# Optimization experiments

Measured on AMD Instinct MI355X. Metric: run time of the kernel, lower is better.

## Reference

```python
import jax, jax.numpy as jnp
import numpy as np

N_X, DIS, IN, OUT = 40000, 10000, 128, 64
N = N_X + DIS
E = 800000
BN_EPS = 1e-5


def setup_inputs() -> dict:
    key = jax.random.key(0)
    ks = jax.random.split(key, 20)

    def glorot(k, shape):
        fan_in, fan_out = shape[-2], shape[-1]
        a = np.sqrt(6.0 / (fan_in + fan_out)).astype(np.float32)
        return jax.random.uniform(k, shape, jnp.float32, -a, a)

    return {
        "x": jax.random.normal(ks[0], (N_X, IN), jnp.float32),
        "emb": jax.random.uniform(ks[1], (DIS, IN), jnp.float32),
        "conv1_w": glorot(ks[2], (3, IN, 2 * OUT)),
        "conv1_root": glorot(ks[3], (IN, 2 * OUT)),
        "conv1_bias": jnp.zeros((2 * OUT,), jnp.float32),
        "conv2_w": glorot(ks[4], (3, 2 * OUT, 4 * OUT)),
        "conv2_root": glorot(ks[5], (2 * OUT, 4 * OUT)),
        "conv2_bias": jnp.zeros((4 * OUT,), jnp.float32),
        "convinf_w": glorot(ks[6], (3, 4 * OUT, 4 * OUT)),
        "convinf_root": glorot(ks[7], (4 * OUT, 4 * OUT)),
        "convinf_bias": jnp.zeros((4 * OUT,), jnp.float32),
        "conv3_w": glorot(ks[8], (3, 4 * OUT, OUT)),
        "conv3_root": glorot(ks[9], (4 * OUT, OUT)),
        "conv3_bias": jnp.zeros((OUT,), jnp.float32),
        "norm1_g": jnp.ones((2 * OUT,), jnp.float32),
        "norm1_b": jnp.zeros((2 * OUT,), jnp.float32),
        "norm2_g": jnp.ones((4 * OUT,), jnp.float32),
        "norm2_b": jnp.zeros((4 * OUT,), jnp.float32),
        "edge_index": jax.random.randint(ks[10], (2, E), 0, N),
        "edge_types": jax.random.randint(ks[11], (E,), 0, 3),
    }


def reference(x, emb, conv1_w, conv1_root, conv1_bias, conv2_w, conv2_root,
              conv2_bias, convinf_w, convinf_root, convinf_bias, conv3_w,
              conv3_root, conv3_bias, norm1_g, norm1_b, norm2_g, norm2_b,
              edge_index, edge_types):
    dst, src = edge_index[0], edge_index[1]  # adj_t row = target, col = source
    n = x.shape[0] + emb.shape[0]

    # gcn_norm without self-loops: deg over rows, w_e = d^-1/2[dst] * d^-1/2[src]
    deg = jax.ops.segment_sum(jnp.ones(dst.shape[0], jnp.float32), dst, num_segments=n)
    dis = jnp.where(deg > 0, jax.lax.rsqrt(jnp.maximum(deg, 1.0)), 0.0)
    ew = dis[dst] * dis[src]  # [E]

    def wrgcn(h, W, root, bias):
        out = h @ root + bias
        h_src = h[src]  # [E, d] gather (dominant memory traffic)
        for r in range(3):
            w_r = jnp.where(edge_types == r, ew, 0.0)
            agg = jax.ops.segment_sum(w_r[:, None] * h_src, dst, num_segments=n)
            out = out + agg @ W[r]
        return out

    def bn(h, g, b):
        m = h.mean(axis=0)
        v = jnp.var(h, axis=0)  # biased, matches torch BN training normalization
        return (h - m) * jax.lax.rsqrt(v + BN_EPS) * g + b

    h0 = jnp.concatenate([x, emb], axis=0)  # [N, IN]
    x1 = bn(wrgcn(h0, conv1_w, conv1_root, conv1_bias), norm1_g, norm1_b)
    x2 = bn(wrgcn(jax.nn.relu(x1), conv2_w, conv2_root, conv2_bias), norm2_g, norm2_b)
    for _ in range(5):
        x2 = bn(wrgcn(jax.nn.relu(x2), convinf_w, convinf_root, convinf_bias), norm2_g, norm2_b)
    return wrgcn(jax.nn.relu(x2), conv3_w, conv3_root, conv3_bias)
```

## Files before the change

### kernel.cpp

```cpp
#include <hip/hip_runtime.h>

#define N_X  40000
#define NN   50000
#define NE   800000
#define MPAD 50048

using short8  = __attribute__((ext_vector_type(8))) short;
using floatx4 = __attribute__((ext_vector_type(4))) float;
using uintx2  = __attribute__((ext_vector_type(2))) unsigned int;
using uintx4  = __attribute__((ext_vector_type(4))) unsigned int;

typedef const __attribute__((address_space(1))) void gv_t;
typedef __attribute__((address_space(3))) void lv_t;

__device__ __forceinline__ unsigned short f2bf(float f) {
  unsigned u = __float_as_uint(f);
  u += 0x7FFF + ((u >> 16) & 1);
  return (unsigned short)(u >> 16);
}
__device__ __forceinline__ float bf2f(unsigned v) {
  return __uint_as_float(v << 16);
}
__device__ __forceinline__ float h2f(unsigned v) {
  unsigned short s = (unsigned short)v;
  _Float16 f;
  __builtin_memcpy(&f, &s, 2);
  return (float)f;
}
__device__ __forceinline__ unsigned short f2h(float f) {
  _Float16 h = (_Float16)f;
  unsigned short s;
  __builtin_memcpy(&s, &h, 2);
  return s;
}

__global__ void k_deg(const int* __restrict__ dst, int* __restrict__ deg) {
  int e = blockIdx.x * blockDim.x + threadIdx.x;
  if (e < NE) atomicAdd(&deg[dst[e]], 1);
}

__global__ void k_dis(const int* __restrict__ deg, float* __restrict__ dis) {
  int i = blockIdx.x * blockDim.x + threadIdx.x;
  if (i < NN) dis[i] = deg[i] > 0 ? rsqrtf((float)deg[i]) : 0.f;
}

#define SCAN_B 1024
#define SCAN_NB 49
__global__ void k_scan1(const int* __restrict__ deg, int* __restrict__ rowp,
                        int* __restrict__ bsum) {
  __shared__ int buf[SCAN_B];
  int b = blockIdx.x;
  int i = b * SCAN_B + threadIdx.x;
  int v = (i < NN) ? deg[i] : 0;
  buf[threadIdx.x] = v;
  __syncthreads();
  for (int off = 1; off < SCAN_B; off <<= 1) {
    int t = (threadIdx.x >= off) ? buf[threadIdx.x - off] : 0;
    __syncthreads();
    buf[threadIdx.x] += t;
    __syncthreads();
  }
  if (i < NN) rowp[i] = buf[threadIdx.x] - v;
  if (threadIdx.x == SCAN_B - 1) bsum[b] = buf[SCAN_B - 1];
}

__global__ void k_scan2(int* __restrict__ bsum) {
  if (threadIdx.x == 0) {
    int acc = 0;
    for (int i = 0; i < SCAN_NB; ++i) { int t = bsum[i]; bsum[i] = acc; acc += t; }
  }
}

__global__ void k_scan3(int* __restrict__ rowp, const int* __restrict__ bsum) {
  int i = blockIdx.x * blockDim.x + threadIdx.x;
  if (i < NN) rowp[i] += bsum[i >> 10];
  if (i == 0) rowp[NN] = NE;
}

__global__ void k_build(const int* __restrict__ dst, const int* __restrict__ src,
                        const int* __restrict__ typ, const float* __restrict__ dis,
                        const int* __restrict__ rowp, int* __restrict__ cur,
                        uintx2* __restrict__ ed) {
  int e = blockIdx.x * blockDim.x + threadIdx.x;
  if (e >= NE) return;
  int d = dst[e], s = src[e];
  int p = rowp[d] + atomicAdd(&cur[d], 1);
  uintx2 v;
  v.x = (unsigned)s | ((unsigned)typ[e] << 28);
  v.y = __float_as_uint(dis[d] * dis[s]);
  ed[p] = v;
}

__global__ void k_prep0(const float* __restrict__ x, const float* __restrict__ emb,
                        unsigned short* __restrict__ Gh, unsigned short* __restrict__ Gl) {
  int idx = blockIdx.x * blockDim.x + threadIdx.x;
  if (idx >= NN * 32) return;
  int r = idx >> 5;
  const float* srcp = (r < N_X) ? (x + (size_t)idx * 4)
                                : (emb + ((size_t)idx - (size_t)N_X * 32) * 4);
  float4 hv = *(const float4*)srcp;
  float vv[4] = {hv.x, hv.y, hv.z, hv.w};
  unsigned hw[2], lw[2];
#pragma unroll
  for (int q = 0; q < 2; ++q) {
    unsigned short h0 = f2bf(vv[2 * q]), h1 = f2bf(vv[2 * q + 1]);
    unsigned short l0 = f2bf(vv[2 * q] - bf2f(h0)), l1 = f2bf(vv[2 * q + 1] - bf2f(h1));
    hw[q] = (unsigned)h0 | ((unsigned)h1 << 16);
    lw[q] = (unsigned)l0 | ((unsigned)l1 << 16);
  }
  size_t o = (size_t)idx * 4;
  *(uintx2*)(Gh + o) = uintx2{hw[0], hw[1]};
  *(uintx2*)(Gl + o) = uintx2{lw[0], lw[1]};
}

__global__ void k_prep(const float* __restrict__ H, const float* __restrict__ sc,
                       const float* __restrict__ sh, unsigned short* __restrict__ Gh,
                       unsigned short* __restrict__ Gl, int din) {
  int idx = blockIdx.x * blockDim.x + threadIdx.x;
  if (idx >= NN * (din >> 2)) return;
  int c4 = (idx & ((din >> 2) - 1)) * 4;
  float4 hv = *(const float4*)(H + (size_t)idx * 4);
  float vv[4] = {hv.x, hv.y, hv.z, hv.w};
#pragma unroll
  for (int q = 0; q < 4; ++q)
    vv[q] = fmaxf(vv[q] * sc[c4 + q] + sh[c4 + q], 0.f);
  unsigned hw[2], lw[2];
#pragma unroll
  for (int q = 0; q < 2; ++q) {
    unsigned short h0 = f2bf(vv[2 * q]), h1 = f2bf(vv[2 * q + 1]);
    unsigned short l0 = f2bf(vv[2 * q] - bf2f(h0)), l1 = f2bf(vv[2 * q + 1] - bf2f(h1));
    hw[q] = (unsigned)h0 | ((unsigned)h1 << 16);
    lw[q] = (unsigned)l0 | ((unsigned)l1 << 16);
  }
  size_t o = (size_t)idx * 4;
  *(uintx2*)(Gh + o) = uintx2{hw[0], hw[1]};
  *(uintx2*)(Gl + o) = uintx2{lw[0], lw[1]};
}

__global__ void k_wcat2(const float* __restrict__ root, const float* __restrict__ W,
                        unsigned short* __restrict__ BhT, unsigned short* __restrict__ BlT,
                        int din, int dout) {
  int idx = blockIdx.x * blockDim.x + threadIdx.x;
  if (idx >= 4 * dout * din) return;
  int n = idx / din, k = idx % din;
  float v;
  if (n < dout) v = root[(size_t)k * dout + n];
  else {
    int r = n / dout - 1, c = n % dout;
    v = W[((size_t)r * din + k) * dout + c];
  }
  unsigned short h = f2bf(v);
  BhT[idx] = h;
  BlT[idx] = f2bf(v - bf2f(h));
}

__global__ __launch_bounds__(256, 2) void k_gemm2(
    const unsigned short* __restrict__ Ah, const unsigned short* __restrict__ Al,
    const unsigned short* __restrict__ Bh, const unsigned short* __restrict__ Bl,
    float* __restrict__ Rroot, unsigned short* __restrict__ P,
    int M, int K, int dout, int ny) {
  constexpr int TC = 40;
  constexpr int CPW = 10;
  constexpr int NT = 2;
  __shared__ __align__(16) char lds[2][TC * 1024];

  const int tid = threadIdx.x;
  const int lane = tid & 63;
  const int w = tid >> 6;
  const int wm = w >> 1, wn = w & 1;
  const int r16 = lane & 15, kg = lane >> 4;

  const int nwg = gridDim.x;
  const int q = nwg >> 3, r = nwg & 7;
  const int xcd = blockIdx.x & 7, pos = blockIdx.x >> 3;
  const int t = (xcd < r ? xcd * (q + 1) : r * (q + 1) + (xcd - r) * q) + pos;
  const int bm = (t / ny) * 256;
  const int bn = (t % ny) * 64;

  const int rowseg = lane >> 2;
  const int seg = (lane & 3) ^ ((lane >> 3) & 3);
  const unsigned short* gb[CPW];
#pragma unroll
  for (int i = 0; i < CPW; ++i) {
    int c = w * CPW + i;
    const unsigned short* base;
    int row0;
    if (c < 16)      { base = Ah; row0 = bm + c * 16; }
    else if (c < 32) { base = Al; row0 = bm + (c - 16) * 16; }
    else if (c < 36) { base = Bh; row0 = bn + (c - 32) * 16; }
    else             { base = Bl; row0 = bn + (c - 36) * 16; }
    gb[i] = base + (size_t)(row0 + rowseg) * K + seg * 8;
  }

  floatx4 acc[8][NT];
#pragma unroll
  for (int i = 0; i < 8; ++i)
#pragma unroll
    for (int jj = 0; jj < NT; ++jj) acc[i][jj] = (floatx4)0.f;

  const int nk = K >> 5;

  auto stage = [&](int b, int tk) {
#pragma unroll
    for (int i = 0; i < CPW; ++i)
      __builtin_amdgcn_global_load_lds((gv_t*)(gb[i] + tk * 32),
                                       (lv_t*)&lds[b][(w * CPW + i) * 1024],
                                       16, 0, 0);
  };

  stage(0, 0);
  stage(1, 1);

  const int fo = r16 * 64 + ((kg ^ ((r16 >> 1) & 3)) * 16);

  int buf = 0;
  for (int tk = 0; tk < nk; ++tk) {
    if (tk < nk - 1) asm volatile("s_waitcnt vmcnt(10)" ::: "memory");
    else             asm volatile("s_waitcnt vmcnt(0)" ::: "memory");
    __builtin_amdgcn_s_barrier();

    const char* Lb = lds[buf];
    short8 bh[NT], bl[NT];
#pragma unroll
    for (int nt = 0; nt < NT; ++nt) {
      bh[nt] = *(const short8*)(Lb + (32 + wn * NT + nt) * 1024 + fo);
      bl[nt] = *(const short8*)(Lb + (36 + wn * NT + nt) * 1024 + fo);
    }

    __builtin_amdgcn_s_setprio(1);
#pragma unroll
    for (int mt = 0; mt < 8; ++mt) {
      short8 ah = *(const short8*)(Lb + (wm * 8 + mt) * 1024 + fo);
      short8 al = *(const short8*)(Lb + (16 + wm * 8 + mt) * 1024 + fo);
#pragma unroll
      for (int nt = 0; nt < NT; ++nt) {
        acc[mt][nt] = __builtin_amdgcn_mfma_f32_16x16x32_bf16(ah, bh[nt], acc[mt][nt], 0, 0, 0);
        acc[mt][nt] = __builtin_amdgcn_mfma_f32_16x16x32_bf16(ah, bl[nt], acc[mt][nt], 0, 0, 0);
        acc[mt][nt] = __builtin_amdgcn_mfma_f32_16x16x32_bf16(al, bh[nt], acc[mt][nt], 0, 0, 0);
      }
    }
    __builtin_amdgcn_s_setprio(0);

    __builtin_amdgcn_s_barrier();
    if (tk + 2 < nk) stage(buf, tk + 2);
    buf ^= 1;
  }

  const int sec = bn / dout;
  const int cb = bn - sec * dout;
#pragma unroll
  for (int mt = 0; mt < 8; ++mt) {
    const int gr0 = bm + wm * 128 + mt * 16 + kg * 4;
#pragma unroll
    for (int nt = 0; nt < NT; ++nt) {
      const int colL = cb + wn * 32 + nt * 16 + r16;
#pragma unroll
      for (int rr = 0; rr < 4; ++rr) {
        const int gr = gr0 + rr;
        if (gr >= M) continue;
        const float o = acc[mt][nt][rr];
        if (sec == 0) Rroot[(size_t)gr * dout + colL] = o;
        else          P[((size_t)gr * 3 + (sec - 1)) * dout + colL] = f2h(o);
      }
    }
  }
}

template <int L>
__global__ void k_agg2(const unsigned short* __restrict__ P,
                       const float* __restrict__ Rroot,
                       const float* __restrict__ bias,
                       const int* __restrict__ rowp, const uintx2* __restrict__ ed,
                       float* __restrict__ Out) {
  constexpr int G = 64 / L;
  constexpr int dout = L * 8;
  const int wid = (blockIdx.x * 256 + threadIdx.x) >> 6;
  if (wid >= NN) return;
  const int lane = threadIdx.x & 63;
  const int grp = lane / L;
  const int c0 = (lane & (L - 1)) * 8;
  const int beg = rowp[wid], end = rowp[wid + 1];
  float a[8] = {};
  for (int i = beg + grp; i < end; i += G) {
    const uintx2 e = ed[i];
    const float wv = __uint_as_float(e.y);
    const unsigned tt = e.x >> 28;
    const size_t off = ((size_t)(e.x & 0x0FFFFFFFu) * 3 + tt) * dout + c0;
    const uintx4 g = *(const uintx4*)(P + off);
    a[0] += wv * h2f(g.x & 0xFFFFu);
    a[1] += wv * h2f(g.x >> 16);
    a[2] += wv * h2f(g.y & 0xFFFFu);
    a[3] += wv * h2f(g.y >> 16);
    a[4] += wv * h2f(g.z & 0xFFFFu);
    a[5] += wv * h2f(g.z >> 16);
    a[6] += wv * h2f(g.w & 0xFFFFu);
    a[7] += wv * h2f(g.w >> 16);
  }
#pragma unroll
  for (int off = L; off < 64; off <<= 1) {
#pragma unroll
    for (int qq = 0; qq < 8; ++qq) a[qq] += __shfl_xor(a[qq], off);
  }
  if (grp == 0) {
    const size_t ob = (size_t)wid * dout + c0;
    const float4 bv0 = *(const float4*)(bias + c0);
    const float4 bv1 = *(const float4*)(bias + c0 + 4);
    const float4 rv0 = *(const float4*)(Rroot + ob);
    const float4 rv1 = *(const float4*)(Rroot + ob + 4);
    float4 o0, o1;
    o0.x = rv0.x + bv0.x + a[0];
    o0.y = rv0.y + bv0.y + a[1];
    o0.z = rv0.z + bv0.z + a[2];
    o0.w = rv0.w + bv0.w + a[3];
    o1.x = rv1.x + bv1.x + a[4];
    o1.y = rv1.y + bv1.y + a[5];
    o1.z = rv1.z + bv1.z + a[6];
    o1.w = rv1.w + bv1.w + a[7];
    *(float4*)(Out + ob) = o0;
    *(float4*)(Out + ob + 4) = o1;
  }
}

__global__ void k_bnstats(const float* __restrict__ H, float* __restrict__ sums, int d) {
  int c = threadIdx.x;
  float s = 0.f, s2 = 0.f;
  for (int r = blockIdx.x; r < NN; r += gridDim.x) {
    float v = H[(size_t)r * d + c];
    s += v;
    s2 += v * v;
  }
  atomicAdd(&sums[c], s);
  atomicAdd(&sums[d + c], s2);
}

__global__ void k_bnfinal(const float* __restrict__ sums, const float* __restrict__ g,
                          const float* __restrict__ b, float* __restrict__ sc,
                          float* __restrict__ sh, int d) {
  int c = threadIdx.x;
  if (c >= d) return;
  float mean = sums[c] * (1.f / NN);
  float var = sums[d + c] * (1.f / NN) - mean * mean;
  float rs = rsqrtf(var + 1e-5f);
  float s = rs * g[c];
  sc[c] = s;
  sh[c] = b[c] - mean * s;
}

extern "C" void kernel_launch(void* const* d_in, const int* in_sizes, int n_in,
                              void* d_out, int out_size, void* d_ws, size_t ws_size,
                              hipStream_t stream) {
  const float* x   = (const float*)d_in[0];
  const float* emb = (const float*)d_in[1];
  const float* conv_w[4] = {(const float*)d_in[2], (const float*)d_in[5],
                            (const float*)d_in[8], (const float*)d_in[11]};
  const float* conv_r[4] = {(const float*)d_in[3], (const float*)d_in[6],
                            (const float*)d_in[9], (const float*)d_in[12]};
  const float* conv_b[4] = {(const float*)d_in[4], (const float*)d_in[7],
                            (const float*)d_in[10], (const float*)d_in[13]};
  const float* n1g = (const float*)d_in[14];
  const float* n1b = (const float*)d_in[15];
  const float* n2g = (const float*)d_in[16];
  const float* n2b = (const float*)d_in[17];
  const int* eidx = (const int*)d_in[18];
  const int* etyp = (const int*)d_in[19];
  const int* dst  = eidx;
  const int* srcp = eidx + NE;
  float* out = (float*)d_out;

  char* w = (char*)d_ws;
  auto alloc = [&](size_t bytes) {
    char* p = w;
    w += (bytes + 255) & ~(size_t)255;
    return p;
  };
  unsigned short* Gh   = (unsigned short*)alloc((size_t)MPAD * 256 * 2);
  unsigned short* Gl   = (unsigned short*)alloc((size_t)MPAD * 256 * 2);
  unsigned short* P    = (unsigned short*)alloc((size_t)MPAD * 768 * 2);
  float*    Rroot = (float*)alloc((size_t)MPAD * 256 * 4);
  float*    H    = (float*)alloc((size_t)NN * 256 * 4);
  unsigned short* WTh[4];
  unsigned short* WTl[4];
  for (int i = 0; i < 4; ++i) {
    WTh[i] = (unsigned short*)alloc((size_t)1024 * 256 * 2);
    WTl[i] = (unsigned short*)alloc((size_t)1024 * 256 * 2);
  }
  float*    bns  = (float*)alloc(512 * 4);
  float*    bsc  = (float*)alloc(256 * 4);
  float*    bsh  = (float*)alloc(256 * 4);
  float*    dis  = (float*)alloc((size_t)NN * 4);
  int*      deg  = (int*)alloc((size_t)NN * 4);
  int*      rowp = (int*)alloc((size_t)(NN + 1) * 4);
  int*      cur  = (int*)alloc((size_t)NN * 4);
  int*      bsum = (int*)alloc(64 * 4);
  uintx2*   ed   = (uintx2*)alloc((size_t)NE * 8);

  hipMemsetAsync(deg, 0, (size_t)NN * 4, stream);
  hipMemsetAsync(cur, 0, (size_t)NN * 4, stream);
  k_deg<<<(NE + 255) / 256, 256, 0, stream>>>(dst, deg);
  k_dis<<<(NN + 255) / 256, 256, 0, stream>>>(deg, dis);
  k_scan1<<<SCAN_NB, SCAN_B, 0, stream>>>(deg, rowp, bsum);
  k_scan2<<<1, 64, 0, stream>>>(bsum);
  k_scan3<<<(NN + 255) / 256, 256, 0, stream>>>(rowp, bsum);
  k_build<<<(NE + 255) / 256, 256, 0, stream>>>(dst, srcp, etyp, dis, rowp, cur, ed);

  const int din_a[8]  = {128, 128, 256, 256, 256, 256, 256, 256};
  const int dout_a[8] = {128, 256, 256, 256, 256, 256, 256, 64};
  const int wi_a[8]   = {0, 1, 2, 2, 2, 2, 2, 3};
  const int gm = (MPAD + 255) / 256;

  const int wdin[4]  = {128, 128, 256, 256};
  const int wdout[4] = {128, 256, 256, 64};
  for (int i = 0; i < 4; ++i)
    k_wcat2<<<(4 * wdout[i] * wdin[i] + 255) / 256, 256, 0, stream>>>(
        conv_r[i], conv_w[i], WTh[i], WTl[i], wdin[i], wdout[i]);

  for (int l = 0; l < 8; ++l) {
    const int din = din_a[l], dout = dout_a[l];
    const int wi = wi_a[l];

    if (l == 0)
      k_prep0<<<(NN * 32 + 255) / 256, 256, 0, stream>>>(x, emb, Gh, Gl);
    else
      k_prep<<<(NN * (din >> 2) + 255) / 256, 256, 0, stream>>>(H, bsc, bsh, Gh, Gl, din);

    const int ny = 4 * dout / 64;
    k_gemm2<<<gm * ny, 256, 0, stream>>>(Gh, Gl, WTh[wi], WTl[wi], Rroot, P, NN, din, dout, ny);

    float* O = (l == 7) ? out : H;
    if (dout == 256)
      k_agg2<32><<<(NN + 3) / 4, 256, 0, stream>>>(P, Rroot, conv_b[wi], rowp, ed, O);
    else if (dout == 128)
      k_agg2<16><<<(NN + 3) / 4, 256, 0, stream>>>(P, Rroot, conv_b[wi], rowp, ed, O);
    else
      k_agg2<8><<<(NN + 3) / 4, 256, 0, stream>>>(P, Rroot, conv_b[wi], rowp, ed, O);

    if (l < 7) {
      hipMemsetAsync(bns, 0, (size_t)2 * dout * 4, stream);
      k_bnstats<<<256, dout, 0, stream>>>(H, bns, dout);
      k_bnfinal<<<1, 256, 0, stream>>>(bns, (l == 0) ? n1g : n2g,
                                       (l == 0) ? n1b : n2b, bsc, bsh, dout);
    }
  }
}
```

Baseline: 1.757 ms.

## Store intermediate layer activations in bf16 and fold BN finalize into prep

Intermediate layer outputs H are now stored as bf16 instead of fp32, which halves write traffic in the aggregation kernel and read traffic in the BN-stats and prep kernels. The separate BN finalize kernel is removed, and each prep thread recomputes mean, variance and scale from the raw sums. Prep is also widened to 8 elements per thread. The cost is lower precision: pre-BN activations are rounded to bf16 before the statistics and normalisation, which may hurt accuracy, and prep does some redundant per-element rsqrt work.

```diff
diff --git a/kernel.cpp b/kernel.cpp
--- a/kernel.cpp
+++ b/kernel.cpp
@@ -113,28 +113,39 @@
   *(uintx2*)(Gl + o) = uintx2{lw[0], lw[1]};
 }
 
-__global__ void k_prep(const float* __restrict__ H, const float* __restrict__ sc,
-                       const float* __restrict__ sh, unsigned short* __restrict__ Gh,
+__global__ void k_prep(const unsigned short* __restrict__ Hb,
+                       const float* __restrict__ bns, const float* __restrict__ g,
+                       const float* __restrict__ b, unsigned short* __restrict__ Gh,
                        unsigned short* __restrict__ Gl, int din) {
   int idx = blockIdx.x * blockDim.x + threadIdx.x;
-  if (idx >= NN * (din >> 2)) return;
-  int c4 = (idx & ((din >> 2) - 1)) * 4;
-  float4 hv = *(const float4*)(H + (size_t)idx * 4);
-  float vv[4] = {hv.x, hv.y, hv.z, hv.w};
-#pragma unroll
-  for (int q = 0; q < 4; ++q)
-    vv[q] = fmaxf(vv[q] * sc[c4 + q] + sh[c4 + q], 0.f);
-  unsigned hw[2], lw[2];
-#pragma unroll
-  for (int q = 0; q < 2; ++q) {
-    unsigned short h0 = f2bf(vv[2 * q]), h1 = f2bf(vv[2 * q + 1]);
-    unsigned short l0 = f2bf(vv[2 * q] - bf2f(h0)), l1 = f2bf(vv[2 * q + 1] - bf2f(h1));
-    hw[q] = (unsigned)h0 | ((unsigned)h1 << 16);
-    lw[q] = (unsigned)l0 | ((unsigned)l1 << 16);
-  }
-  size_t o = (size_t)idx * 4;
-  *(uintx2*)(Gh + o) = uintx2{hw[0], hw[1]};
-  *(uintx2*)(Gl + o) = uintx2{lw[0], lw[1]};
+  if (idx >= NN * (din >> 3)) return;
+  int c8 = (idx & ((din >> 3) - 1)) * 8;
+  uintx4 hv = *(const uintx4*)(Hb + (size_t)idx * 8);
+  unsigned hwv[4] = {hv.x, hv.y, hv.z, hv.w};
+  unsigned hw[4], lw[4];
+#pragma unroll
+  for (int q = 0; q < 4; ++q) {
+    unsigned short oo[2];
+#pragma unroll
+    for (int p = 0; p < 2; ++p) {
+      int c = c8 + 2 * q + p;
+      float mean = bns[c] * (1.f / NN);
+      float var = bns[din + c] * (1.f / NN) - mean * mean;
+      float rs = rsqrtf(var + 1e-5f);
+      float sc = rs * g[c];
+      float sh = b[c] - mean * sc;
+      float v = bf2f((hwv[q] >> (16 * p)) & 0xFFFFu);
+      v = fmaxf(v * sc + sh, 0.f);
+      oo[p] = f2bf(v);
+      float lo = v - bf2f(oo[p]);
+      if (p == 0) lw[q] = (unsigned)f2bf(lo);
+      else        lw[q] |= ((unsigned)f2bf(lo) << 16);
+    }
+    hw[q] = (unsigned)oo[0] | ((unsigned)oo[1] << 16);
+  }
+  size_t o = (size_t)idx * 8;
+  *(uintx4*)(Gh + o) = uintx4{hw[0], hw[1], hw[2], hw[3]};
+  *(uintx4*)(Gl + o) = uintx4{lw[0], lw[1], lw[2], lw[3]};
 }
 
 __global__ void k_wcat2(const float* __restrict__ root, const float* __restrict__ W,
@@ -266,12 +277,12 @@
   }
 }
 
-template <int L>
+template <int L, bool F32OUT>
 __global__ void k_agg2(const unsigned short* __restrict__ P,
                        const float* __restrict__ Rroot,
                        const float* __restrict__ bias,
                        const int* __restrict__ rowp, const uintx2* __restrict__ ed,
-                       float* __restrict__ Out) {
+                       void* __restrict__ OutV) {
   constexpr int G = 64 / L;
   constexpr int dout = L * 8;
   const int wid = (blockIdx.x * 256 + threadIdx.x) >> 6;
@@ -307,43 +318,42 @@
     const float4 bv1 = *(const float4*)(bias + c0 + 4);
     const float4 rv0 = *(const float4*)(Rroot + ob);
     const float4 rv1 = *(const float4*)(Rroot + ob + 4);
-    float4 o0, o1;
-    o0.x = rv0.x + bv0.x + a[0];
-    o0.y = rv0.y + bv0.y + a[1];
-    o0.z = rv0.z + bv0.z + a[2];
-    o0.w = rv0.w + bv0.w + a[3];
-    o1.x = rv1.x + bv1.x + a[4];
-    o1.y = rv1.y + bv1.y + a[5];
-    o1.z = rv1.z + bv1.z + a[6];
-    o1.w = rv1.w + bv1.w + a[7];
-    *(float4*)(Out + ob) = o0;
-    *(float4*)(Out + ob + 4) = o1;
-  }
-}
-
-__global__ void k_bnstats(const float* __restrict__ H, float* __restrict__ sums, int d) {
+    float o[8];
+    o[0] = rv0.x + bv0.x + a[0];
+    o[1] = rv0.y + bv0.y + a[1];
+    o[2] = rv0.z + bv0.z + a[2];
+    o[3] = rv0.w + bv0.w + a[3];
+    o[4] = rv1.x + bv1.x + a[4];
+    o[5] = rv1.y + bv1.y + a[5];
+    o[6] = rv1.z + bv1.z + a[6];
+    o[7] = rv1.w + bv1.w + a[7];
+    if constexpr (F32OUT) {
+      float* Out = (float*)OutV;
+      *(float4*)(Out + ob) = make_float4(o[0], o[1], o[2], o[3]);
+      *(float4*)(Out + ob + 4) = make_float4(o[4], o[5], o[6], o[7]);
+    } else {
+      unsigned short* Out = (unsigned short*)OutV;
+      uintx4 pk;
+      pk.x = (unsigned)f2bf(o[0]) | ((unsigned)f2bf(o[1]) << 16);
+      pk.y = (unsigned)f2bf(o[2]) | ((unsigned)f2bf(o[3]) << 16);
+      pk.z = (unsigned)f2bf(o[4]) | ((unsigned)f2bf(o[5]) << 16);
+      pk.w = (unsigned)f2bf(o[6]) | ((unsigned)f2bf(o[7]) << 16);
+      *(uintx4*)(Out + ob) = pk;
+    }
+  }
+}
+
+__global__ void k_bnstats(const unsigned short* __restrict__ Hb,
+                          float* __restrict__ sums, int d) {
   int c = threadIdx.x;
   float s = 0.f, s2 = 0.f;
   for (int r = blockIdx.x; r < NN; r += gridDim.x) {
-    float v = H[(size_t)r * d + c];
+    float v = bf2f(Hb[(size_t)r * d + c]);
     s += v;
     s2 += v * v;
   }
   atomicAdd(&sums[c], s);
   atomicAdd(&sums[d + c], s2);
-}
-
-__global__ void k_bnfinal(const float* __restrict__ sums, const float* __restrict__ g,
-                          const float* __restrict__ b, float* __restrict__ sc,
-                          float* __restrict__ sh, int d) {
-  int c = threadIdx.x;
-  if (c >= d) return;
-  float mean = sums[c] * (1.f / NN);
-  float var = sums[d + c] * (1.f / NN) - mean * mean;
-  float rs = rsqrtf(var + 1e-5f);
-  float s = rs * g[c];
-  sc[c] = s;
-  sh[c] = b[c] - mean * s;
 }
 
 extern "C" void kernel_launch(void* const* d_in, const int* in_sizes, int n_in,
@@ -377,7 +387,7 @@
   unsigned short* Gl   = (unsigned short*)alloc((size_t)MPAD * 256 * 2);
   unsigned short* P    = (unsigned short*)alloc((size_t)MPAD * 768 * 2);
   float*    Rroot = (float*)alloc((size_t)MPAD * 256 * 4);
-  float*    H    = (float*)alloc((size_t)NN * 256 * 4);
+  unsigned short* Hb = (unsigned short*)alloc((size_t)NN * 256 * 2);
   unsigned short* WTh[4];
   unsigned short* WTl[4];
   for (int i = 0; i < 4; ++i) {
@@ -385,8 +395,6 @@
     WTl[i] = (unsigned short*)alloc((size_t)1024 * 256 * 2);
   }
   float*    bns  = (float*)alloc(512 * 4);
-  float*    bsc  = (float*)alloc(256 * 4);
-  float*    bsh  = (float*)alloc(256 * 4);
   float*    dis  = (float*)alloc((size_t)NN * 4);
   int*      deg  = (int*)alloc((size_t)NN * 4);
   int*      rowp = (int*)alloc((size_t)(NN + 1) * 4);
@@ -421,24 +429,21 @@
     if (l == 0)
       k_prep0<<<(NN * 32 + 255) / 256, 256, 0, stream>>>(x, emb, Gh, Gl);
     else
-      k_prep<<<(NN * (din >> 2) + 255) / 256, 256, 0, stream>>>(H, bsc, bsh, Gh, Gl, din);
+      k_prep<<<(NN * (din >> 3) + 255) / 256, 256, 0, stream>>>(
+          Hb, bns, (l == 1) ? n1g : n2g, (l == 1) ? n1b : n2b, Gh, Gl, din);
 
     const int ny = 4 * dout / 64;
     k_gemm2<<<gm * ny, 256, 0, stream>>>(Gh, Gl, WTh[wi], WTl[wi], Rroot, P, NN, din, dout, ny);
 
-    float* O = (l == 7) ? out : H;
-    if (dout == 256)
-      k_agg2<32><<<(NN + 3) / 4, 256, 0, stream>>>(P, Rroot, conv_b[wi], rowp, ed, O);
-    else if (dout == 128)
-      k_agg2<16><<<(NN + 3) / 4, 256, 0, stream>>>(P, Rroot, conv_b[wi], rowp, ed, O);
-    else
-      k_agg2<8><<<(NN + 3) / 4, 256, 0, stream>>>(P, Rroot, conv_b[wi], rowp, ed, O);
-
-    if (l < 7) {
+    if (l == 7) {
+      k_agg2<8, true><<<(NN + 3) / 4, 256, 0, stream>>>(P, Rroot, conv_b[wi], rowp, ed, out);
+    } else {
+      if (dout == 256)
+        k_agg2<32, false><<<(NN + 3) / 4, 256, 0, stream>>>(P, Rroot, conv_b[wi], rowp, ed, Hb);
+      else
+        k_agg2<16, false><<<(NN + 3) / 4, 256, 0, stream>>>(P, Rroot, conv_b[wi], rowp, ed, Hb);
       hipMemsetAsync(bns, 0, (size_t)2 * dout * 4, stream);
-      k_bnstats<<<256, dout, 0, stream>>>(H, bns, dout);
-      k_bnfinal<<<1, 256, 0, stream>>>(bns, (l == 0) ? n1g : n2g,
-                                       (l == 0) ? n1b : n2b, bsc, bsh, dout);
-    }
-  }
-}
+      k_bnstats<<<256, dout, 0, stream>>>(Hb, bns, dout);
+    }
+  }
+}
```

After: 1.711 ms. -2.7%, faster.
